# Performance work log

Measured on AMD Instinct MI355X. Metric: run time of the kernel, lower is better.

The kernel has to match this reference:

```python
import jax, jax.numpy as jnp
import numpy as np

N, D, NS, HID = 65536, 256, 1024, 256
EPS = 1e-8
SCALE = D ** -0.5


def layer_norm(x, w, b, eps=1e-5):
    mu = jnp.mean(x, axis=-1, keepdims=True)
    var = jnp.mean(jnp.square(x - mu), axis=-1, keepdims=True)
    return (x - mu) * jax.lax.rsqrt(var + eps) * w + b


def mask_attn(attn, k):
    # per-row top-k mask, vectorized (replaces the torch Python loop)
    idx = jax.lax.top_k(attn, k)[1]                      # [rows, k]
    rows = jnp.arange(attn.shape[0])[:, None]
    mask = jnp.zeros(attn.shape, jnp.bool_).at[rows, idx].set(True)
    return attn * mask


def setup_inputs() -> dict:
    key = jax.random.key(0)
    ks = jax.random.split(key, 20)
    def lin_w(k, din, dout):
        return jax.random.normal(k, (din, dout), jnp.float32) * (1.0 / np.sqrt(din))
    return {
        "inputs": jax.random.normal(ks[0], (N, D), jnp.float32),
        "noise": jax.random.normal(ks[1], (NS, D), jnp.float32),
        "edges_mu": jax.random.normal(ks[2], (1, D), jnp.float32),
        "edges_logsigma": jax.random.uniform(ks[3], (1, D), jnp.float32, -0.1, 0.1),
        "wq": lin_w(ks[4], D, D), "bq": jnp.zeros((D,), jnp.float32),
        "wk": lin_w(ks[5], D, D), "bk": jnp.zeros((D,), jnp.float32),
        "wv": lin_w(ks[6], D, D), "bv": jnp.zeros((D,), jnp.float32),
        "mlp_w1": lin_w(ks[7], 2 * D, HID), "mlp_b1": jnp.zeros((HID,), jnp.float32),
        "mlp_w2": lin_w(ks[8], HID, D), "mlp_b2": jnp.zeros((D,), jnp.float32),
        "ln_in_w": jnp.ones((D,), jnp.float32), "ln_in_b": jnp.zeros((D,), jnp.float32),
        "ln_e_w": jnp.ones((D,), jnp.float32), "ln_e_b": jnp.zeros((D,), jnp.float32),
        "k_n": 512,
        "k_e": 32,
    }


def reference(inputs, noise, edges_mu, edges_logsigma, wq, bq, wk, bk, wv, bv,
              mlp_w1, mlp_b1, mlp_w2, mlp_b2, ln_in_w, ln_in_b, ln_e_w, ln_e_b,
              k_n, k_e):
    # slot init: mu + sigma * eps
    edges = edges_mu + jnp.exp(edges_logsigma) * noise            # [NS, D]
    x = layer_norm(inputs, ln_in_w, ln_in_b)                      # [N, D]
    k = jax.nn.relu(x @ wk + bk)                                  # [N, D]
    v = jax.nn.relu(x @ wv + bv)                                  # [N, D]

    # iters = 1 (single unrolled iteration, as in the default config)
    e = layer_norm(edges, ln_e_w, ln_e_b)                         # [NS, D]
    q = jax.nn.relu(e @ wq + bq)                                  # [NS, D]
    dots = (q @ k.T) * SCALE                                      # [NS, N]
    attn = jax.nn.softmax(dots, axis=1) + EPS
    attn = attn / jnp.sum(attn, axis=1, keepdims=True)
    attn = mask_attn(attn, k_n)
    updates = attn @ v                                            # [NS, D]
    edges = jax.nn.relu(jnp.concatenate([e, updates], axis=1) @ mlp_w1 + mlp_b1) @ mlp_w2 + mlp_b2  # [NS, D]

    q2 = x @ wq + bq                                              # [N, D] (no relu, as in source)
    k2 = jax.nn.relu(edges @ wk + bk)                             # [NS, D]
    dots2 = (q2 @ k2.T) * SCALE                                   # [N, NS]
    H = mask_attn(jax.nn.softmax(dots2, axis=1), k_e)             # [N, NS]
    return edges, H, dots2
```

## Files before the change

### kernel.cpp

```cpp
#include <hip/hip_runtime.h>
#include <hip/hip_bf16.h>
#include <stdint.h>


#define DEV __device__ __forceinline__

typedef uint32_t u32;
typedef uint16_t u16;
typedef __bf16 v8bf __attribute__((ext_vector_type(8)));
typedef float v4f __attribute__((ext_vector_type(4)));

static constexpr long NN = 65536;
static constexpr long DD = 256;
static constexpr long NSL = 1024;

DEV u16 f2b(float f) {
  u32 u = __builtin_bit_cast(u32, f);
  u32 r = (u + 0x7FFFu + ((u >> 16) & 1u)) >> 16;
  return (u16)r;
}
DEV float b2f(u16 h) { u32 u = ((u32)h) << 16; return __builtin_bit_cast(float, u); }
DEV u32 b2k(u32 b) { return b ^ (0x8000u + 0x7FFFu * (b >> 15)); }
DEV float k2fv(u32 k) {
  u16 b = (k & 0x8000u) ? (u16)(k ^ 0x8000u) : (u16)(k ^ 0xFFFFu);
  return b2f(b);
}

DEV void gl_lds16(const u16* g, u16* l) {
  __builtin_amdgcn_global_load_lds(
      (const __attribute__((address_space(1))) u32*)g,
      (__attribute__((address_space(3))) u32*)l, 16, 0, 0);
}

template <int EPI>
__global__ __launch_bounds__(256, 2)
void gemm_bt(const u16* __restrict__ A, const u16* __restrict__ B,
             const float* __restrict__ bias, float scale,
             u16* __restrict__ ob0, u16* __restrict__ ob1, u16* __restrict__ ob2,
             float* __restrict__ of) {
  __shared__ __align__(16) u16 As[128 * 64];
  __shared__ __align__(16) u16 Bs[128 * 64];
  const int tid = threadIdx.x;
  const int lane = tid & 63;
  const int l15 = lane & 15;
  const int l4 = lane >> 4;
  const int wid = tid >> 6;
  const int wm = wid >> 1, wn = wid & 1;
  const long m0 = (long)blockIdx.y * 128;
  const long n0 = (long)blockIdx.x * 128;

  v4f acc[4][4] = {};

  for (int kb = 0; kb < 256; kb += 64) {
    __syncthreads();
#pragma unroll
    for (int i = 0; i < 4; i++) {
      int cid = tid + 256 * i;
      int row = cid >> 3, ch = cid & 7;
      int sch = ch ^ (row & 7);
      gl_lds16(A + (m0 + row) * 256 + kb + sch * 8, &As[cid * 8]);
      gl_lds16(B + (n0 + row) * 256 + kb + sch * 8, &Bs[cid * 8]);
    }
    __syncthreads();
#pragma unroll
    for (int ks = 0; ks < 2; ks++) {
      v8bf af[4], bfr[4];
#pragma unroll
      for (int m = 0; m < 4; m++) {
        int row = wm * 64 + m * 16 + l15;
        int sch = (ks * 4 + l4) ^ (row & 7);
        af[m] = *reinterpret_cast<const v8bf*>(&As[row * 64 + sch * 8]);
      }
#pragma unroll
      for (int n = 0; n < 4; n++) {
        int row = wn * 64 + n * 16 + l15;
        int sch = (ks * 4 + l4) ^ (row & 7);
        bfr[n] = *reinterpret_cast<const v8bf*>(&Bs[row * 64 + sch * 8]);
      }
#pragma unroll
      for (int m = 0; m < 4; m++)
#pragma unroll
        for (int n = 0; n < 4; n++)
          acc[m][n] = __builtin_amdgcn_mfma_f32_16x16x32_bf16(af[m], bfr[n], acc[m][n], 0, 0, 0);
    }
  }

  const int r4 = l4 * 4;
#pragma unroll
  for (int m = 0; m < 4; m++) {
#pragma unroll
    for (int n = 0; n < 4; n++) {
#pragma unroll
      for (int r = 0; r < 4; r++) {
        long grow = m0 + wm * 64 + m * 16 + r4 + r;
        long gcol = n0 + wn * 64 + n * 16 + l15;
        float v = acc[m][n][r];
        if constexpr (EPI == 0) {
          v += bias[gcol];
          int which = (int)(gcol >> 8);
          long jj = gcol & 255;
          if (which < 2) v = fmaxf(v, 0.f);
          u16 hv = f2b(v);
          if (which == 0) ob0[grow * 256 + jj] = hv;
          else if (which == 1) ob1[grow * 256 + jj] = hv;
          else ob2[grow * 256 + jj] = hv;
        } else if constexpr (EPI == 1) {
          v += bias[gcol];
          v = fmaxf(v, 0.f);
          ob0[grow * 256 + gcol] = f2b(v);
        } else if constexpr (EPI == 2) {
          ob0[grow * 65536 + gcol] = f2b(v * scale);
        } else {
          of[grow * 1024 + gcol] = v * scale;
        }
      }
    }
  }
}

__global__ __launch_bounds__(256)
void prep_w_kernel(const float* __restrict__ wq, const float* __restrict__ wk,
                   const float* __restrict__ wv, const float* __restrict__ bq,
                   const float* __restrict__ bk, const float* __restrict__ bv,
                   u16* __restrict__ wcat, float* __restrict__ bcat) {
  int n = blockIdx.x;
  int t = threadIdx.x;
  const float* W = (n < 256) ? wk : (n < 512) ? wv : wq;
  int jj = n & 255;
  wcat[n * 256 + t] = f2b(W[t * 256 + jj]);
  if (t == 0) {
    const float* Bb = (n < 256) ? bk : (n < 512) ? bv : bq;
    bcat[n] = Bb[jj];
  }
}

__global__ __launch_bounds__(256)
void ln_x_kernel(const float* __restrict__ x, const float* __restrict__ lw,
                 const float* __restrict__ lb, u16* __restrict__ out) {
  const int lane = threadIdx.x & 63, wid = threadIdx.x >> 6;
  const long row = (long)blockIdx.x * 4 + wid;
  float4 v = reinterpret_cast<const float4*>(x + row * 256)[lane];
  float s = v.x + v.y + v.z + v.w;
  for (int sh = 1; sh < 64; sh <<= 1) s += __shfl_xor(s, sh);
  float mu = s * (1.f / 256.f);
  float dx = v.x - mu, dy = v.y - mu, dz = v.z - mu, dw = v.w - mu;
  float q = dx * dx + dy * dy + dz * dz + dw * dw;
  for (int sh = 1; sh < 64; sh <<= 1) q += __shfl_xor(q, sh);
  float rs = rsqrtf(q * (1.f / 256.f) + 1e-5f);
  float4 wv = reinterpret_cast<const float4*>(lw)[lane];
  float4 bv = reinterpret_cast<const float4*>(lb)[lane];
  ushort4 o4;
  o4.x = f2b(dx * rs * wv.x + bv.x);
  o4.y = f2b(dy * rs * wv.y + bv.y);
  o4.z = f2b(dz * rs * wv.z + bv.z);
  o4.w = f2b(dw * rs * wv.w + bv.w);
  reinterpret_cast<ushort4*>(out + row * 256)[lane] = o4;
}

__global__ __launch_bounds__(256)
void edges_e_kernel(const float* __restrict__ noise, const float* __restrict__ emu,
                    const float* __restrict__ els, const float* __restrict__ lw,
                    const float* __restrict__ lb, float* __restrict__ e_f,
                    u16* __restrict__ e_b) {
  const int lane = threadIdx.x & 63, wid = threadIdx.x >> 6;
  const long row = (long)blockIdx.x * 4 + wid;
  float4 nz = reinterpret_cast<const float4*>(noise + row * 256)[lane];
  float4 mu4 = reinterpret_cast<const float4*>(emu)[lane];
  float4 ls4 = reinterpret_cast<const float4*>(els)[lane];
  float4 ed;
  ed.x = mu4.x + expf(ls4.x) * nz.x;
  ed.y = mu4.y + expf(ls4.y) * nz.y;
  ed.z = mu4.z + expf(ls4.z) * nz.z;
  ed.w = mu4.w + expf(ls4.w) * nz.w;
  float s = ed.x + ed.y + ed.z + ed.w;
  for (int sh = 1; sh < 64; sh <<= 1) s += __shfl_xor(s, sh);
  float mu = s * (1.f / 256.f);
  float dx = ed.x - mu, dy = ed.y - mu, dz = ed.z - mu, dw = ed.w - mu;
  float qv = dx * dx + dy * dy + dz * dz + dw * dw;
  for (int sh = 1; sh < 64; sh <<= 1) qv += __shfl_xor(qv, sh);
  float rs = rsqrtf(qv * (1.f / 256.f) + 1e-5f);
  float4 wv = reinterpret_cast<const float4*>(lw)[lane];
  float4 bv = reinterpret_cast<const float4*>(lb)[lane];
  float4 ef;
  ef.x = dx * rs * wv.x + bv.x;
  ef.y = dy * rs * wv.y + bv.y;
  ef.z = dz * rs * wv.z + bv.z;
  ef.w = dw * rs * wv.w + bv.w;
  reinterpret_cast<float4*>(e_f + row * 256)[lane] = ef;
  ushort4 o4;
  o4.x = f2b(ef.x); o4.y = f2b(ef.y); o4.z = f2b(ef.z); o4.w = f2b(ef.w);
  reinterpret_cast<ushort4*>(e_b + row * 256)[lane] = o4;
}

struct D2Shm {
  u32 hist[256 * 16];
  u32 c_hi[256];
  u32 sel_idx[1152];
  float sel_w[1152];
  float fred[4];
  u32 sb_star, sThi, sThr;
  float sSE, sFrac;
  u32 scnt;
};

__global__ __launch_bounds__(256, 5)
void d2d3_kernel(const u16* __restrict__ dots, const u16* __restrict__ vmat,
                 const int* __restrict__ knp, float* __restrict__ upd) {
  __shared__ D2Shm S;
  const int tid = threadIdx.x, lane = tid & 63, wid = tid >> 6;
  const int hc = (lane >> 2);
  const long r = blockIdx.x;
  const int kn = *knp;

  for (int i = tid; i < 4096; i += 256) S.hist[i] = 0;
  if (tid == 0) S.scnt = 0;
  __syncthreads();

  const float C = 8.f;
  const uint4* src = reinterpret_cast<const uint4*>(dots + r * 65536);

  float se = 0.f;
  for (int c = tid; c < 8192; c += 256) {
    uint4 d = src[c];
    u32 h[8] = {d.x & 0xffffu, d.x >> 16, d.y & 0xffffu, d.y >> 16,
                d.z & 0xffffu, d.z >> 16, d.w & 0xffffu, d.w >> 16};
#pragma unroll
    for (int j = 0; j < 8; j++) {
      u32 k = b2k(h[j]);
      se += __expf(b2f((u16)h[j]) - C);
      atomicAdd(&S.hist[(k >> 8) * 16 + hc], 1u);
    }
  }
  for (int sh = 1; sh < 64; sh <<= 1) se += __shfl_xor(se, sh);
  if (lane == 0) S.fred[wid] = se;
  __syncthreads();

  {
    u32 s = 0;
#pragma unroll
    for (int c = 0; c < 16; c++) s += S.hist[tid * 16 + c];
    S.c_hi[tid] = s;
  }
  __syncthreads();

  if (tid < 64) {
    u32 s = S.c_hi[4 * tid] + S.c_hi[4 * tid + 1] + S.c_hi[4 * tid + 2] + S.c_hi[4 * tid + 3];
    u32 v = s;
    for (int off = 1; off < 64; off <<= 1) {
      u32 t = (u32)__shfl_down((int)v, off);
      if (tid + off < 64) v += t;
    }
    u32 excl = v - s;
    if (v >= (u32)kn && excl < (u32)kn) {
      u32 acc = excl;
#pragma unroll
      for (int bb = 3; bb >= 0; --bb) {
        int b = 4 * tid + bb;
        u32 nb = acc + S.c_hi[b];
        if (nb >= (u32)kn) { S.sb_star = (u32)b; S.sThi = acc; break; }
        acc = nb;
      }
    }
  } else {
    for (int i = tid - 64; i < 4096; i += 192) S.hist[i] = 0;
  }
  __syncthreads();
  const u32 bstar = S.sb_star;

  for (int c = tid; c < 8192; c += 256) {
    uint4 d = src[c];
    u32 h[8] = {d.x & 0xffffu, d.x >> 16, d.y & 0xffffu, d.y >> 16,
                d.z & 0xffffu, d.z >> 16, d.w & 0xffffu, d.w >> 16};
#pragma unroll
    for (int j = 0; j < 8; j++) {
      u32 k = b2k(h[j]);
      if ((k >> 8) == bstar) atomicAdd(&S.hist[(k & 255u) * 16 + hc], 1u);
    }
  }
  __syncthreads();
  {
    u32 s = 0;
#pragma unroll
    for (int c = 0; c < 16; c++) s += S.hist[tid * 16 + c];
    S.c_hi[tid] = s;
  }
  __syncthreads();

  if (tid < 64) {
    u32 s = S.c_hi[4 * tid] + S.c_hi[4 * tid + 1] + S.c_hi[4 * tid + 2] + S.c_hi[4 * tid + 3];
    u32 v = s;
    for (int off = 1; off < 64; off <<= 1) {
      u32 t = (u32)__shfl_down((int)v, off);
      if (tid + off < 64) v += t;
    }
    const u32 Thi = S.sThi;
    u32 incl = v + Thi;
    u32 excl = v - s + Thi;
    if (incl >= (u32)kn && excl < (u32)kn) {
      u32 acc = excl;
#pragma unroll
      for (int bb = 3; bb >= 0; --bb) {
        int b = 4 * tid + bb;
        u32 nb = acc + S.c_hi[b];
        if (nb >= (u32)kn) {
          S.sThr = (bstar << 8) | (u32)b;
          S.sFrac = (float)(int)((u32)kn - acc) / (float)S.c_hi[b];
          break;
        }
        acc = nb;
      }
    }
    if (tid == 0) {
      float SE = S.fred[0] + S.fred[1] + S.fred[2] + S.fred[3];
      S.sSE = SE;
    }
  }
  __syncthreads();
  const u32 thr = S.sThr;
  const float frac = S.sFrac;
  const float invs = 1.f / S.sSE;
  const float wnorm = 1.f / (1.f + 65536.f * 1e-8f);

  for (int c = tid; c < 8192; c += 256) {
    uint4 d = src[c];
    u32 h[8] = {d.x & 0xffffu, d.x >> 16, d.y & 0xffffu, d.y >> 16,
                d.z & 0xffffu, d.z >> 16, d.w & 0xffffu, d.w >> 16};
#pragma unroll
    for (int j = 0; j < 8; j++) {
      u32 k = b2k(h[j]);
      if (k >= thr) {
        float w = (__expf(k2fv(k) - C) * invs + 1e-8f) * wnorm;
        if (k == thr) w *= frac;
        u32 p = atomicAdd(&S.scnt, 1u);
        if (p < 1152u) { S.sel_idx[p] = (u32)c * 8u + (u32)j; S.sel_w[p] = w; }
      }
    }
  }
  __syncthreads();
  const u32 nsel = S.scnt < 1152u ? S.scnt : 1152u;

  float a0 = 0.f, a1 = 0.f, a2 = 0.f, a3 = 0.f;
  u32 j = 0;
  for (; j + 3 < nsel; j += 4) {
    a0 = fmaf(S.sel_w[j], b2f(vmat[(long)S.sel_idx[j] * 256 + tid]), a0);
    a1 = fmaf(S.sel_w[j + 1], b2f(vmat[(long)S.sel_idx[j + 1] * 256 + tid]), a1);
    a2 = fmaf(S.sel_w[j + 2], b2f(vmat[(long)S.sel_idx[j + 2] * 256 + tid]), a2);
    a3 = fmaf(S.sel_w[j + 3], b2f(vmat[(long)S.sel_idx[j + 3] * 256 + tid]), a3);
  }
  for (; j < nsel; ++j)
    a0 = fmaf(S.sel_w[j], b2f(vmat[(long)S.sel_idx[j] * 256 + tid]), a0);
  upd[r * 256 + tid] = (a0 + a1) + (a2 + a3);
}

__global__ __launch_bounds__(256)
void mlp_kernel(const float* __restrict__ e, const float* __restrict__ upd,
                const float* __restrict__ w1, const float* __restrict__ b1,
                const float* __restrict__ w2, const float* __restrict__ b2,
                float* __restrict__ eout, u16* __restrict__ eb) {
  __shared__ float ecat[512];
  __shared__ float h[256];
  const int t = threadIdx.x;
  const long r = blockIdx.x;
  ecat[t] = e[r * 256 + t];
  ecat[256 + t] = upd[r * 256 + t];
  __syncthreads();
  float acc = b1[t];
#pragma unroll 8
  for (int kk = 0; kk < 512; ++kk) acc = fmaf(ecat[kk], w1[kk * 256 + t], acc);
  h[t] = fmaxf(acc, 0.f);
  __syncthreads();
  float a2 = b2[t];
#pragma unroll 8
  for (int kk = 0; kk < 256; ++kk) a2 = fmaf(h[kk], w2[kk * 256 + t], a2);
  eout[r * 256 + t] = a2;
  eb[r * 256 + t] = f2b(a2);
}

__global__ __launch_bounds__(256)
void g2_kernel(const float* __restrict__ d2, const int* __restrict__ kep,
               float* __restrict__ H) {
  const int lane = threadIdx.x & 63, wid = threadIdx.x >> 6;
  const long row = (long)blockIdx.x * 4 + wid;
  const int ke = *kep;
  const float4* src = reinterpret_cast<const float4*>(d2 + row * 1024);
  float4 q0 = src[lane], q1 = src[64 + lane], q2v = src[128 + lane], q3 = src[192 + lane];
  float x[16] = {q0.x, q0.y, q0.z, q0.w, q1.x, q1.y, q1.z, q1.w,
                 q2v.x, q2v.y, q2v.z, q2v.w, q3.x, q3.y, q3.z, q3.w};
  float mx = x[0];
#pragma unroll
  for (int i = 1; i < 16; i++) mx = fmaxf(mx, x[i]);
  for (int sh = 1; sh < 64; sh <<= 1) mx = fmaxf(mx, __shfl_xor(mx, sh));
  float p[16];
  float se = 0.f;
#pragma unroll
  for (int i = 0; i < 16; i++) { p[i] = __expf(x[i] - mx); se += p[i]; }
  for (int sh = 1; sh < 64; sh <<= 1) se += __shfl_xor(se, sh);
  const float invs = 1.f / se;
  u32 key[16];
#pragma unroll
  for (int i = 0; i < 16; i++) {
    u32 u = __builtin_bit_cast(u32, x[i]);
    key[i] = u ^ ((u >> 31) ? 0xFFFFFFFFu : 0x80000000u);
  }
  u32 lo = 0;
  for (int b = 31; b >= 0; --b) {
    u32 t = lo | (1u << b);
    int cnt = 0;
#pragma unroll
    for (int i = 0; i < 16; i++) cnt += (key[i] >= t);
    for (int sh = 1; sh < 64; sh <<= 1) cnt += __shfl_xor(cnt, sh);
    if (cnt >= ke) lo = t;
  }
  float4 o0, o1, o2, o3;
  o0.x = key[0] >= lo ? p[0] * invs : 0.f;
  o0.y = key[1] >= lo ? p[1] * invs : 0.f;
  o0.z = key[2] >= lo ? p[2] * invs : 0.f;
  o0.w = key[3] >= lo ? p[3] * invs : 0.f;
  o1.x = key[4] >= lo ? p[4] * invs : 0.f;
  o1.y = key[5] >= lo ? p[5] * invs : 0.f;
  o1.z = key[6] >= lo ? p[6] * invs : 0.f;
  o1.w = key[7] >= lo ? p[7] * invs : 0.f;
  o2.x = key[8] >= lo ? p[8] * invs : 0.f;
  o2.y = key[9] >= lo ? p[9] * invs : 0.f;
  o2.z = key[10] >= lo ? p[10] * invs : 0.f;
  o2.w = key[11] >= lo ? p[11] * invs : 0.f;
  o3.x = key[12] >= lo ? p[12] * invs : 0.f;
  o3.y = key[13] >= lo ? p[13] * invs : 0.f;
  o3.z = key[14] >= lo ? p[14] * invs : 0.f;
  o3.w = key[15] >= lo ? p[15] * invs : 0.f;
  float4* dst = reinterpret_cast<float4*>(H + row * 1024);
  dst[lane] = o0;
  dst[64 + lane] = o1;
  dst[128 + lane] = o2;
  dst[192 + lane] = o3;
}

extern "C" void kernel_launch(void* const* d_in, const int* in_sizes, int n_in,
                              void* d_out, int out_size, void* d_ws, size_t ws_size,
                              hipStream_t stream) {
  (void)in_sizes; (void)n_in; (void)out_size; (void)ws_size;

  float* out = (float*)d_out;
  float* out_edges = out;
  float* out_H = out + NSL * DD;
  float* out_d2 = out_H + NN * NSL;

  char* Hb = (char*)out_H;
  u16* dots = (u16*)Hb;
  u16* q2b = (u16*)(Hb + 134217728L);
  char* smb = Hb + 167772160L;
  u16* wcat = (u16*)smb;      smb += 768 * 256 * 2;
  float* bcat = (float*)smb;  smb += 4096;
  float* e_f = (float*)smb;   smb += 1024 * 256 * 4;
  u16* e_b = (u16*)smb;       smb += 1024 * 256 * 2;
  u16* q_b = (u16*)smb;       smb += 1024 * 256 * 2;
  float* updf = (float*)smb;  smb += 1024 * 256 * 4;
  u16* edg_b = (u16*)smb;     smb += 1024 * 256 * 2;
  char* Db = (char*)out_d2;
  u16* xln = (u16*)Db;
  u16* kb_ = (u16*)(Db + 33554432L);
  u16* vb_ = (u16*)(Db + 67108864L);
  u16* k2ws = (u16*)d_ws;

  prep_w_kernel<<<768, 256, 0, stream>>>(
      (const float*)d_in[4], (const float*)d_in[6], (const float*)d_in[8],
      (const float*)d_in[5], (const float*)d_in[7], (const float*)d_in[9], wcat, bcat);
  edges_e_kernel<<<256, 256, 0, stream>>>(
      (const float*)d_in[1], (const float*)d_in[2], (const float*)d_in[3],
      (const float*)d_in[16], (const float*)d_in[17], e_f, e_b);
  ln_x_kernel<<<16384, 256, 0, stream>>>(
      (const float*)d_in[0], (const float*)d_in[14], (const float*)d_in[15], xln);
  gemm_bt<1><<<dim3(2, 8), 256, 0, stream>>>(e_b, wcat + 512 * 256, bcat + 512, 1.f,
                                             q_b, nullptr, nullptr, nullptr);
  gemm_bt<0><<<dim3(6, 512), 256, 0, stream>>>(xln, wcat, bcat, 1.f,
                                               kb_, vb_, q2b, nullptr);
  gemm_bt<2><<<dim3(512, 8), 256, 0, stream>>>(q_b, kb_, nullptr, 0.0625f,
                                               dots, nullptr, nullptr, nullptr);
  d2d3_kernel<<<1024, 256, 0, stream>>>(dots, vb_, (const int*)d_in[18], updf);
  mlp_kernel<<<1024, 256, 0, stream>>>(e_f, updf,
                                       (const float*)d_in[10], (const float*)d_in[11],
                                       (const float*)d_in[12], (const float*)d_in[13],
                                       out_edges, edg_b);
  gemm_bt<1><<<dim3(2, 8), 256, 0, stream>>>(edg_b, wcat, bcat, 1.f,
                                             k2ws, nullptr, nullptr, nullptr);
  gemm_bt<3><<<dim3(8, 512), 256, 0, stream>>>(q2b, k2ws, nullptr, 0.0625f,
                                               nullptr, nullptr, nullptr, out_d2);
  g2_kernel<<<16384, 256, 0, stream>>>(out_d2, (const int*)d_in[19], out_H);
}
```

Before: 594.5 us.

## Vectorize update gather across waves; use bf16 keys for row top-k search

The update kernel now splits the selected rows across the four waves. Each thread loads four bf16 columns at once with ushort4, and the per-wave partial sums are combined through shared memory. This replaces one scalar 2-byte gather per thread per selected row. The per-row top-k_e threshold search in the H kernel now rounds logits to bf16 sortable keys, so the bitwise binary search runs 16 passes, each with a wave-wide shuffle reduction, instead of 32. The risk is that ties after bf16 rounding can admit more than k_e entries into the mask, which makes the selection differ slightly from exact float top-k.

```diff
diff --git a/kernel.cpp b/kernel.cpp
--- a/kernel.cpp
+++ b/kernel.cpp
@@ -339,17 +339,34 @@
   __syncthreads();
   const u32 nsel = S.scnt < 1152u ? S.scnt : 1152u;
 
+  const int g = tid >> 6;
+  const int c0 = (tid & 63) * 4;
   float a0 = 0.f, a1 = 0.f, a2 = 0.f, a3 = 0.f;
-  u32 j = 0;
-  for (; j + 3 < nsel; j += 4) {
-    a0 = fmaf(S.sel_w[j], b2f(vmat[(long)S.sel_idx[j] * 256 + tid]), a0);
-    a1 = fmaf(S.sel_w[j + 1], b2f(vmat[(long)S.sel_idx[j + 1] * 256 + tid]), a1);
-    a2 = fmaf(S.sel_w[j + 2], b2f(vmat[(long)S.sel_idx[j + 2] * 256 + tid]), a2);
-    a3 = fmaf(S.sel_w[j + 3], b2f(vmat[(long)S.sel_idx[j + 3] * 256 + tid]), a3);
-  }
-  for (; j < nsel; ++j)
-    a0 = fmaf(S.sel_w[j], b2f(vmat[(long)S.sel_idx[j] * 256 + tid]), a0);
-  upd[r * 256 + tid] = (a0 + a1) + (a2 + a3);
+  float b0 = 0.f, b1 = 0.f, b2 = 0.f, b3 = 0.f;
+  u32 j = (u32)g;
+  for (; j + 4 < nsel; j += 8) {
+    u32 i0 = S.sel_idx[j];      float w0 = S.sel_w[j];
+    u32 i1 = S.sel_idx[j + 4];  float w1 = S.sel_w[j + 4];
+    ushort4 v0 = *reinterpret_cast<const ushort4*>(vmat + (long)i0 * 256 + c0);
+    ushort4 v1 = *reinterpret_cast<const ushort4*>(vmat + (long)i1 * 256 + c0);
+    a0 = fmaf(w0, b2f(v0.x), a0); a1 = fmaf(w0, b2f(v0.y), a1);
+    a2 = fmaf(w0, b2f(v0.z), a2); a3 = fmaf(w0, b2f(v0.w), a3);
+    b0 = fmaf(w1, b2f(v1.x), b0); b1 = fmaf(w1, b2f(v1.y), b1);
+    b2 = fmaf(w1, b2f(v1.z), b2); b3 = fmaf(w1, b2f(v1.w), b3);
+  }
+  for (; j < nsel; j += 4) {
+    u32 i0 = S.sel_idx[j];  float w0 = S.sel_w[j];
+    ushort4 v0 = *reinterpret_cast<const ushort4*>(vmat + (long)i0 * 256 + c0);
+    a0 = fmaf(w0, b2f(v0.x), a0); a1 = fmaf(w0, b2f(v0.y), a1);
+    a2 = fmaf(w0, b2f(v0.z), a2); a3 = fmaf(w0, b2f(v0.w), a3);
+  }
+  __syncthreads();
+  float* part = reinterpret_cast<float*>(S.hist);
+  float4 pv;
+  pv.x = a0 + b0; pv.y = a1 + b1; pv.z = a2 + b2; pv.w = a3 + b3;
+  *reinterpret_cast<float4*>(&part[g * 256 + c0]) = pv;
+  __syncthreads();
+  upd[r * 256 + tid] = part[tid] + part[256 + tid] + part[512 + tid] + part[768 + tid];
 }
 
 __global__ __launch_bounds__(256)
@@ -398,12 +415,9 @@
   const float invs = 1.f / se;
   u32 key[16];
 #pragma unroll
-  for (int i = 0; i < 16; i++) {
-    u32 u = __builtin_bit_cast(u32, x[i]);
-    key[i] = u ^ ((u >> 31) ? 0xFFFFFFFFu : 0x80000000u);
-  }
+  for (int i = 0; i < 16; i++) key[i] = b2k((u32)f2b(x[i]));
   u32 lo = 0;
-  for (int b = 31; b >= 0; --b) {
+  for (int b = 15; b >= 0; --b) {
     u32 t = lo | (1u << b);
     int cnt = 0;
 #pragma unroll
```

Measured after the change: 517.0 us. -13.0%, faster.
